# Kernel optimization log

Hardware: AMD Instinct MI355X
Metric: run time of the kernel (lower is better)

Reference implementation:

```python
import jax, jax.numpy as jnp
import numpy as np

EMB = 128     # embedding_size
HEADS = 4     # n_heads
LAYERS = 2    # n_layers
T = 10        # number of graphs / timesteps (== window_size)
N = 20000     # nodes per graph
E = 320000    # edges per graph
B = 4096      # clf_nodes
WIN = 10      # window_size
NEG_SLOPE = 0.2


def setup_inputs() -> dict:
    key = jax.random.key(0)
    ks = jax.random.split(key, 26)
    p = lambda k, shape: 0.05 * jax.random.normal(k, shape, jnp.float32)
    inp = {
        "embeddings": jax.random.normal(ks[0], (T, N, EMB), jnp.float32),
        "edges": jax.random.randint(ks[1], (T, 2, E), 0, N),
        "node_type": jax.random.randint(ks[2], (T, N), 0, 4),
        "edge_type": jax.random.randint(ks[3], (T, E), 0, 4),
        "clf_neighbors": jax.random.randint(ks[4], (B,), 0, N),
        "clf_nodes": jax.random.randint(ks[5], (B,), 0, N),
        # branch 1 GAT stacks: lin weight [L, H*C, D], attention vecs [L, H, C], bias [L, H*C]
        "gat_W1": p(ks[6], (LAYERS, HEADS * EMB, EMB)),
        "gat_as1": p(ks[7], (LAYERS, HEADS, EMB)),
        "gat_ad1": p(ks[8], (LAYERS, HEADS, EMB)),
        "gat_b1": p(ks[9], (LAYERS, HEADS * EMB)),
        "lin_W1": p(ks[10], (LAYERS, EMB, HEADS * EMB)),
        "lin_b1": p(ks[11], (LAYERS, EMB)),
        # branch 2
        "gat_W2": p(ks[12], (LAYERS, HEADS * EMB, EMB)),
        "gat_as2": p(ks[13], (LAYERS, HEADS, EMB)),
        "gat_ad2": p(ks[14], (LAYERS, HEADS, EMB)),
        "gat_b2": p(ks[15], (LAYERS, HEADS * EMB)),
        "lin_W2": p(ks[16], (LAYERS, EMB, HEADS * EMB)),
        "lin_b2": p(ks[17], (LAYERS, EMB)),
        # head MLP (fc1 consumes flattened [window * 2*D])
        "fc1_W": p(ks[18], (EMB, 2 * EMB * WIN)),
        "fc1_b": p(ks[19], (EMB,)),
        "fc2_W": p(ks[20], (2, EMB)),
        "fc2_b": p(ks[21], (2,)),
    }
    return inp


def _gat(x, src, dst, W, a_s, a_d, b):
    """PyG-style GATConv (concat=True, self-loops already in src/dst, eval mode)."""
    n = x.shape[0]
    h = (x @ W.T).reshape(n, HEADS, EMB)                       # [N,H,C]
    logits = jax.nn.leaky_relu((h * a_s).sum(-1)[src] + (h * a_d).sum(-1)[dst], NEG_SLOPE)  # [Etot,H]
    logits = logits - jax.ops.segment_max(logits, dst, num_segments=n)[dst]
    ex = jnp.exp(logits)
    alpha = ex / jax.ops.segment_sum(ex, dst, num_segments=n)[dst]  # segment softmax over targets
    out = jax.ops.segment_sum(alpha[:, :, None] * h[src], dst, num_segments=n)  # [N,H,C]
    return out.reshape(n, HEADS * EMB) + b


def _branch(embeddings, edges, gW, gas, gad, gb, lW, lb):
    loops = jnp.arange(N)

    def step(carry, inputs):
        x, edge = inputs
        src = jnp.concatenate([edge[0], loops])  # add self loops (PyG default)
        dst = jnp.concatenate([edge[1], loops])
        for i in range(LAYERS):
            x = _gat(x, src, dst, gW[i], gas[i], gad[i], gb[i])
            x = jax.nn.relu(x @ lW[i].T + lb[i])
        return carry, x

    _, outs = jax.lax.scan(step, 0, (embeddings, edges))
    return outs  # [T,N,EMB]


def reference(embeddings, edges, node_type, edge_type, clf_neighbors, clf_nodes,
              gat_W1, gat_as1, gat_ad1, gat_b1, lin_W1, lin_b1,
              gat_W2, gat_as2, gat_ad2, gat_b2, lin_W2, lin_b2,
              fc1_W, fc1_b, fc2_W, fc2_b):
    o1 = _branch(embeddings, edges, gat_W1, gat_as1, gat_ad1, gat_b1, lin_W1, lin_b1)
    o2 = _branch(embeddings, edges, gat_W2, gat_as2, gat_ad2, gat_b2, lin_W2, lin_b2)
    # original prepends each graph's output -> reversed timestep order
    e1 = o1[::-1][:, clf_nodes].transpose(1, 0, 2)  # [B,T,EMB]
    e2 = o2[::-1][:, clf_nodes].transpose(1, 0, 2)
    temp = jnp.concatenate([e1, e2], axis=2)        # [B,T,2*EMB]
    # slen == window_size -> skip buffer is fully filled by temp
    flat = temp.reshape(temp.shape[0], WIN * 2 * EMB)
    h = jax.nn.relu(flat @ fc1_W.T + fc1_b)
    return jax.nn.relu(h @ fc2_W.T + fc2_b)        # [B,2]
```

## Files before the change

### kernel.cpp

```cpp
#include <hip/hip_runtime.h>
#include <cstdint>

#define NNODES 20000
#define NEDGES 320000
#define ETOT   340000
#define TSTEPS 10
#define BCLF   4096
#define EMB    128
#define HC     512
#define NEG_SLOPE 0.2f

#define NSB    64
#define SBSPAN 313
#define PCAP   6912
#define ECHUNK 2048
#define NCHUNKS ((NEDGES + ECHUNK - 1) / ECHUNK)
#define NSCHUNK ((NNODES + 255) / 256)
#define STAGECAP 7424

typedef _Float16 half_t;
typedef __attribute__((ext_vector_type(8))) _Float16 half8;
typedef __attribute__((ext_vector_type(4))) float floatx4;

__global__ void cvt_split_kernel(const float* __restrict__ in,
                                 half_t* __restrict__ hi, half_t* __restrict__ lo, long n4) {
    long i = (long)blockIdx.x * 256 + threadIdx.x;
    if (i >= n4) return;
    float4 v = *(const float4*)&in[i * 4];
    half_t h[4], l[4];
    h[0] = (half_t)v.x; l[0] = (half_t)(v.x - (float)h[0]);
    h[1] = (half_t)v.y; l[1] = (half_t)(v.y - (float)h[1]);
    h[2] = (half_t)v.z; l[2] = (half_t)(v.z - (float)h[2]);
    h[3] = (half_t)v.w; l[3] = (half_t)(v.w - (float)h[3]);
    *(unsigned long long*)&hi[i * 4] = *(unsigned long long*)h;
    *(unsigned long long*)&lo[i * 4] = *(unsigned long long*)l;
}

__global__ __launch_bounds__(256) void part64_kernel(const int* __restrict__ edges,
                                                     int* __restrict__ bcnt,
                                                     int* __restrict__ pairs) {
    int g = blockIdx.y;
    int c = blockIdx.x;
    __shared__ int hist[NSB], gbase[NSB], cur[NSB];
    if (threadIdx.x < NSB) hist[threadIdx.x] = 0;
    __syncthreads();
    const int* srcp = edges + (long)g * 2 * NEDGES;
    const int* dstp = srcp + NEDGES;
    int e0 = c * ECHUNK + threadIdx.x;
    int s[8], d[8], sb[8];
#pragma unroll
    for (int i = 0; i < 8; i++) {
        int e = e0 + i * 256;
        if (e < NEDGES) {
            s[i] = srcp[e];
            d[i] = dstp[e];
            sb[i] = (int)((unsigned)d[i] / (unsigned)SBSPAN);
            atomicAdd(&hist[sb[i]], 1);
        } else sb[i] = -1;
    }
    __syncthreads();
    if (threadIdx.x < NSB) {
        int h = hist[threadIdx.x];
        gbase[threadIdx.x] = h ? atomicAdd(&bcnt[g * NSB + threadIdx.x], h) : 0;
        cur[threadIdx.x] = 0;
    }
    __syncthreads();
#pragma unroll
    for (int i = 0; i < 8; i++) {
        if (sb[i] >= 0) {
            int pos = gbase[sb[i]] + atomicAdd(&cur[sb[i]], 1);
            int v = s[i] | ((d[i] - sb[i] * SBSPAN) << 15);
            pairs[((long)(g * NSB + sb[i])) * PCAP + pos] = v;
        }
    }
}

__global__ __launch_bounds__(256) void count_sb_kernel(const int* __restrict__ pairs,
                                                       const int* __restrict__ bcnt,
                                                       int* __restrict__ counts) {
    int g = blockIdx.x >> 6, sb = blockIdx.x & 63;
    __shared__ int hist[SBSPAN];
    for (int i = threadIdx.x; i < SBSPAN; i += 256) hist[i] = 0;
    __syncthreads();
    int n0 = sb * SBSPAN;
    int cnt = bcnt[g * NSB + sb];
    const int* p = pairs + (long)(g * NSB + sb) * PCAP;
    for (int k = threadIdx.x; k < cnt; k += 256)
        atomicAdd(&hist[p[k] >> 15], 1);
    __syncthreads();
    int nn = min(SBSPAN, NNODES - n0);
    for (int i = threadIdx.x; i < nn; i += 256)
        counts[g * NNODES + n0 + i] = hist[i];
}

__global__ void scanA_kernel(const int* __restrict__ counts, int* __restrict__ bsum) {
    int g = blockIdx.x / NSCHUNK, ch = blockIdx.x % NSCHUNK;
    int i = ch * 256 + threadIdx.x;
    int v = (i < NNODES) ? counts[g * NNODES + i] + 1 : 0;
    for (int off = 32; off; off >>= 1) v += __shfl_down(v, off);
    __shared__ int ws[4];
    if ((threadIdx.x & 63) == 0) ws[threadIdx.x >> 6] = v;
    __syncthreads();
    if (threadIdx.x == 0) bsum[blockIdx.x] = ws[0] + ws[1] + ws[2] + ws[3];
}

__global__ void scanB_kernel(const int* __restrict__ bsum, int* __restrict__ boff,
                             int* __restrict__ rowptr) {
    int g = blockIdx.x;
    int tid = threadIdx.x;
    int v = (tid < NSCHUNK) ? bsum[g * NSCHUNK + tid] : 0;
    __shared__ int buf[128];
    buf[tid] = v;
    __syncthreads();
    for (int off = 1; off < 128; off <<= 1) {
        int t = (tid >= off) ? buf[tid - off] : 0;
        __syncthreads();
        buf[tid] += t;
        __syncthreads();
    }
    if (tid < NSCHUNK) boff[g * NSCHUNK + tid] = buf[tid] - v;
    if (tid == 127) rowptr[g * (NNODES + 1) + NNODES] = buf[127];
}

__global__ void scanC_kernel(const int* __restrict__ counts, const int* __restrict__ boff,
                             int* __restrict__ rowptr) {
    int g = blockIdx.x / NSCHUNK, ch = blockIdx.x % NSCHUNK;
    int tid = threadIdx.x;
    int i = ch * 256 + tid;
    int v = (i < NNODES) ? counts[g * NNODES + i] + 1 : 0;
    __shared__ int buf[256];
    buf[tid] = v;
    __syncthreads();
    for (int off = 1; off < 256; off <<= 1) {
        int t = (tid >= off) ? buf[tid - off] : 0;
        __syncthreads();
        buf[tid] += t;
        __syncthreads();
    }
    int excl = boff[blockIdx.x] + buf[tid] - v;
    if (i < NNODES) rowptr[g * (NNODES + 1) + i] = excl;
}

__global__ __launch_bounds__(256) void fill_sb_kernel(const int* __restrict__ pairs,
                                                      const int* __restrict__ bcnt,
                                                      const int* __restrict__ rowptr,
                                                      int* __restrict__ csr_src) {
    int g = blockIdx.x >> 6, sb = blockIdx.x & 63;
    __shared__ int cur[SBSPAN];
    __shared__ int stage[STAGECAP];
    int n0 = sb * SBSPAN;
    int nn = min(SBSPAN, NNODES - n0);
    const int* rp = rowptr + g * (NNODES + 1);
    int base = rp[n0];
    int span = rp[n0 + nn] - base;
    for (int i = threadIdx.x; i < nn; i += 256) {
        int rb = rp[n0 + i] - base;
        stage[rb] = n0 + i;
        cur[i] = rb + 1;
    }
    __syncthreads();
    int cnt = bcnt[g * NSB + sb];
    const int* p = pairs + (long)(g * NSB + sb) * PCAP;
    for (int k = threadIdx.x; k < cnt; k += 256) {
        int v = p[k];
        int pos = atomicAdd(&cur[v >> 15], 1);
        stage[pos] = v & 0x7fff;
    }
    __syncthreads();
    int* dst = csr_src + (long)g * ETOT + base;
    for (int k = threadIdx.x; k < span; k += 256) dst[k] = stage[k];
}

__global__ void prep_was_kernel(const float* __restrict__ W1, const float* __restrict__ W2,
                                const float* __restrict__ as1, const float* __restrict__ as2,
                                const float* __restrict__ ad1, const float* __restrict__ ad2,
                                float* __restrict__ was, float* __restrict__ wad) {
    int b = blockIdx.x;
    int l = b >> 3, z = (b >> 2) & 1, h = b & 3;
    int k = threadIdx.x;
    const float* W  = z ? W2 : W1;
    const float* av = z ? as2 : as1;
    const float* dv = z ? ad2 : ad1;
    float s = 0.f, d = 0.f;
    for (int c = 0; c < 128; c++) {
        float w = W[(long)l * HC * EMB + (h * 128 + c) * 128 + k];
        s = fmaf(w, av[(l * 4 + h) * 128 + c], s);
        d = fmaf(w, dv[(l * 4 + h) * 128 + c], d);
    }
    long idx = ((l * 2 + z) * 4 + h) * 128 + k;
    was[idx] = s;
    wad[idx] = d;
}

__global__ void pack_ws_kernel(const float* __restrict__ wasb, const float* __restrict__ wadb,
                               half_t* __restrict__ WS0h, half_t* __restrict__ WS0l,
                               half_t* __restrict__ WS1h, half_t* __restrict__ WS1l) {
    int b = blockIdx.x;
    int k = threadIdx.x;
    if (b < 16) {
        int z = b >> 3, d = (b >> 2) & 1, h = b & 3;
        const float* src = d ? wadb : wasb;
        float v = src[((long)z * 4 + h) * 128 + k];
        half_t hi = (half_t)v;
        WS0h[b * 128 + k] = hi;
        WS0l[b * 128 + k] = (half_t)(v - (float)hi);
    } else {
        int b2 = b - 16;
        int z = b2 >> 4, r = b2 & 15;
        float v = 0.f;
        if (r < 8) {
            int d = r >> 2, h = r & 3;
            const float* src = d ? wadb : wasb;
            v = src[((long)(2 + z) * 4 + h) * 128 + k];
        }
        half_t hi = (half_t)v;
        WS1h[(z * 16 + r) * 128 + k] = hi;
        WS1l[(z * 16 + r) * 128 + k] = (half_t)(v - (float)hi);
    }
}

__global__ void prep_M_kernel(const float* __restrict__ gW1, const float* __restrict__ gW2,
                              const float* __restrict__ lW1, const float* __restrict__ lW2,
                              half_t* __restrict__ Mh, half_t* __restrict__ Ml) {
    int k = blockIdx.x;
    int inst = blockIdx.y;
    int l = inst >> 1, z = inst & 1;
    int c = threadIdx.x;
    const float* gW = (z ? gW2 : gW1) + (long)l * HC * EMB;
    const float* lW = (z ? lW2 : lW1) + (long)l * EMB * HC;
    float acc[4] = {0.f, 0.f, 0.f, 0.f};
    for (int cp = 0; cp < 128; cp++) {
#pragma unroll
        for (int h = 0; h < 4; h++) {
            float lw = lW[(long)k * 512 + h * 128 + cp];
            float gw = gW[(long)(h * 128 + cp) * 128 + c];
            acc[h] = fmaf(lw, gw, acc[h]);
        }
    }
#pragma unroll
    for (int h = 0; h < 4; h++) {
        long o = ((long)inst * 128 + k) * 512 + h * 128 + c;
        half_t hi = (half_t)acc[h];
        Mh[o] = hi;
        Ml[o] = (half_t)(acc[h] - (float)hi);
    }
}

__global__ void prep_cb_kernel(const float* __restrict__ lW1, const float* __restrict__ lW2,
                               const float* __restrict__ gb1_, const float* __restrict__ gb2_,
                               const float* __restrict__ lb1_, const float* __restrict__ lb2_,
                               float* __restrict__ cb) {
    int inst = blockIdx.x;
    int l = inst >> 1, z = inst & 1;
    int k = threadIdx.x;
    const float* lW = (z ? lW2 : lW1) + (long)l * EMB * HC;
    const float* gb = (z ? gb2_ : gb1_) + l * HC;
    const float* lb = (z ? lb2_ : lb1_) + l * EMB;
    float a = lb[k];
    for (int j = 0; j < 512; j++) a = fmaf(lW[(long)k * 512 + j], gb[j], a);
    cb[inst * 128 + k] = a;
}

__global__ __launch_bounds__(256) void scores_b(
    const half_t* __restrict__ Ahb, const half_t* __restrict__ Alb, long aInst,
    const half_t* __restrict__ WShb, const half_t* __restrict__ WSlb, long wInst, int wMask,
    float* __restrict__ outb, long oInst, int M, int OS, int CMAX) {
    int iy = blockIdx.y;
    const half_t* Ah = Ahb + (long)iy * aInst;
    const half_t* Al = Alb + (long)iy * aInst;
    const half_t* WSh = WShb + (long)(iy & wMask) * wInst;
    const half_t* WSl = WSlb + (long)(iy & wMask) * wInst;
    float* out = outb + (long)iy * oInst;
    __shared__ half_t Bh[16 * 128];
    __shared__ half_t Bl[16 * 128];
    int tid = threadIdx.x;
    *(half8*)&Bh[tid * 8] = *(const half8*)&WSh[tid * 8];
    *(half8*)&Bl[tid * 8] = *(const half8*)&WSl[tid * 8];
    __syncthreads();
    int wave = tid >> 6, lane = tid & 63;
    int l16 = lane & 15, chunk = lane >> 4;
    int r0 = blockIdx.x * 64 + wave * 16;
    int rowc = r0 + l16; if (rowc > M - 1) rowc = M - 1;
    floatx4 acc = (floatx4)0.f;
#pragma unroll
    for (int ko = 0; ko < 128; ko += 32) {
        half8 ah = *(const half8*)&Ah[(long)rowc * 128 + ko + chunk * 8];
        half8 al = *(const half8*)&Al[(long)rowc * 128 + ko + chunk * 8];
        half8 bh = *(const half8*)&Bh[l16 * 128 + ko + chunk * 8];
        half8 bl = *(const half8*)&Bl[l16 * 128 + ko + chunk * 8];
        acc = __builtin_amdgcn_mfma_f32_16x16x32_f16(ah, bh, acc, 0, 0, 0);
        acc = __builtin_amdgcn_mfma_f32_16x16x32_f16(ah, bl, acc, 0, 0, 0);
        acc = __builtin_amdgcn_mfma_f32_16x16x32_f16(al, bh, acc, 0, 0, 0);
    }
#pragma unroll
    for (int reg = 0; reg < 4; reg++) {
        int rr = r0 + chunk * 4 + reg;
        if (rr < M && l16 < CMAX) out[(long)rr * OS + l16] = acc[reg];
    }
}

__global__ __launch_bounds__(256) void agg_x_kernel(
    const half_t* __restrict__ Xb, long xsT, long xsG,
    const float* __restrict__ ssb, int stsh, long ssT, long ssG, int zcol,
    const int* __restrict__ rowptr, const int* __restrict__ csr_src,
    half_t* __restrict__ Yh, half_t* __restrict__ Yl, int t0) {
    int tz = blockIdx.z, t = t0 + tz, z = blockIdx.y;
    int gz = tz * 2 + z;
    int n = blockIdx.x * 4 + (threadIdx.x >> 6);
    int lane = threadIdx.x & 63;
    int h = lane >> 4, cg = lane & 15;
    const int* rp = rowptr + t * (NNODES + 1);
    int beg = rp[n], end = rp[n + 1];
    const int* cs = csr_src + (long)t * ETOT;
    const half_t* Xz = Xb + (long)t * xsT + (long)gz * xsG;
    const float* sz = ssb + (long)t * ssT + (long)gz * ssG + (long)z * zcol;
    float sd = sz[((long)n << stsh) + 4 + h];
    float acc[8];
#pragma unroll
    for (int c = 0; c < 8; c++) acc[c] = 0.f;
    float den = 0.f;

    auto proc4 = [&](int s0, int s1, int s2, int s3) {
        float v0 = sz[((long)s0 << stsh) + h];
        float v1 = sz[((long)s1 << stsh) + h];
        float v2 = sz[((long)s2 << stsh) + h];
        float v3 = sz[((long)s3 << stsh) + h];
        half8 x0 = *(const half8*)&Xz[(long)s0 * 128 + cg * 8];
        half8 x1 = *(const half8*)&Xz[(long)s1 * 128 + cg * 8];
        half8 x2 = *(const half8*)&Xz[(long)s2 * 128 + cg * 8];
        half8 x3 = *(const half8*)&Xz[(long)s3 * 128 + cg * 8];
        float L0 = v0 + sd, L1 = v1 + sd, L2 = v2 + sd, L3 = v3 + sd;
        float w0 = __expf(fmaxf(L0, NEG_SLOPE * L0));
        float w1 = __expf(fmaxf(L1, NEG_SLOPE * L1));
        float w2 = __expf(fmaxf(L2, NEG_SLOPE * L2));
        float w3 = __expf(fmaxf(L3, NEG_SLOPE * L3));
        den += (w0 + w1) + (w2 + w3);
#pragma unroll
        for (int c = 0; c < 8; c++) {
            float a = acc[c];
            a = fmaf(w0, (float)x0[c], a);
            a = fmaf(w1, (float)x1[c], a);
            a = fmaf(w2, (float)x2[c], a);
            a = fmaf(w3, (float)x3[c], a);
            acc[c] = a;
        }
    };

    int j = beg;
    int rem = end - beg;
    if (rem >= 8) {
        int a0 = cs[j], a1 = cs[j + 1], a2 = cs[j + 2], a3 = cs[j + 3];
        while (j + 8 <= end) {
            int b0 = cs[j + 4], b1 = cs[j + 5], b2 = cs[j + 6], b3 = cs[j + 7];
            proc4(a0, a1, a2, a3);
            a0 = b0; a1 = b1; a2 = b2; a3 = b3;
            j += 4;
        }
        proc4(a0, a1, a2, a3);
        j += 4;
    } else if (rem >= 4) {
        proc4(cs[j], cs[j + 1], cs[j + 2], cs[j + 3]);
        j += 4;
    }
    for (; j < end; j++) {
        int src = cs[j];
        float sv = sz[((long)src << stsh) + h];
        half8 x = *(const half8*)&Xz[(long)src * 128 + cg * 8];
        float L = sv + sd;
        float w = __expf(fmaxf(L, NEG_SLOPE * L));
        den += w;
#pragma unroll
        for (int c = 0; c < 8; c++) acc[c] = fmaf(w, (float)x[c], acc[c]);
    }
    float inv = 1.0f / den;
    half8 oh, ol;
#pragma unroll
    for (int c = 0; c < 8; c++) {
        float v = acc[c] * inv;
        half_t hi = (half_t)v;
        oh[c] = hi;
        ol[c] = (half_t)(v - (float)hi);
    }
    long yb = ((long)gz * NNODES + n) * 512 + h * 128 + cg * 8;
    *(half8*)&Yh[yb] = oh;
    *(half8*)&Yl[yb] = ol;
}

__global__ __launch_bounds__(256) void gemm_b(
    const half_t* __restrict__ Ahb, const half_t* __restrict__ Alb, long aInst,
    const half_t* __restrict__ Bhb, const half_t* __restrict__ Blb, long bInst,
    const float* __restrict__ biasb, long biasInst,
    half_t* __restrict__ Ch, half_t* __restrict__ Cl,
    long cInst, int M, int N, int K) {
    const int i = blockIdx.z;
    const half_t* __restrict__ Ah = Ahb + (long)i * aInst;
    const half_t* __restrict__ Al = Alb + (long)i * aInst;
    const half_t* __restrict__ Bh = Bhb + (long)(i & 1) * bInst;
    const half_t* __restrict__ Bl = Blb + (long)(i & 1) * bInst;
    const float* __restrict__ bias = biasb + (long)(i & 1) * biasInst;

    __shared__ half_t Ash[4 * 128 * 8];
    __shared__ half_t Asl[4 * 128 * 8];
    __shared__ half_t Bsh[4 * 128 * 8];
    __shared__ half_t Bsl[4 * 128 * 8];

    const int tid = threadIdx.x;
    const int row0 = blockIdx.x * 128;
    const int col0 = blockIdx.y * 128;
    const int wave = tid >> 6;
    const int lane = tid & 63;
    const int wm = (wave >> 1) * 64;
    const int wn = (wave & 1) * 64;
    const int chunk = lane >> 4;
    const int l16 = lane & 15;

    floatx4 acc[4][4];
#pragma unroll
    for (int ii = 0; ii < 4; ii++)
#pragma unroll
        for (int j = 0; j < 4; j++) acc[ii][j] = (floatx4)0.0f;

    for (int k0 = 0; k0 < K; k0 += 32) {
        __syncthreads();
#pragma unroll
        for (int p = 0; p < 2; p++) {
            int idx = p * 256 + tid;
            int r = idx >> 2, kc = idx & 3;
            int arow = row0 + r;
            half8 vah, val;
            if (arow < M) {
                vah = *(const half8*)&Ah[(long)arow * K + k0 + kc * 8];
                val = *(const half8*)&Al[(long)arow * K + k0 + kc * 8];
            } else {
#pragma unroll
                for (int q = 0; q < 8; q++) { vah[q] = (half_t)0.f; val[q] = (half_t)0.f; }
            }
            *(half8*)&Ash[(kc * 128 + r) * 8] = vah;
            *(half8*)&Asl[(kc * 128 + r) * 8] = val;
            long boff = (long)(col0 + r) * K + k0 + kc * 8;
            *(half8*)&Bsh[(kc * 128 + r) * 8] = *(const half8*)&Bh[boff];
            *(half8*)&Bsl[(kc * 128 + r) * 8] = *(const half8*)&Bl[boff];
        }
        __syncthreads();
        half8 afh[4], afl[4], bfh[4], bfl[4];
#pragma unroll
        for (int mi = 0; mi < 4; mi++) {
            int o = (chunk * 128 + wm + mi * 16 + l16) * 8;
            afh[mi] = *(const half8*)&Ash[o];
            afl[mi] = *(const half8*)&Asl[o];
        }
#pragma unroll
        for (int ni = 0; ni < 4; ni++) {
            int o = (chunk * 128 + wn + ni * 16 + l16) * 8;
            bfh[ni] = *(const half8*)&Bsh[o];
            bfl[ni] = *(const half8*)&Bsl[o];
        }
#pragma unroll
        for (int mi = 0; mi < 4; mi++)
#pragma unroll
            for (int ni = 0; ni < 4; ni++) {
                acc[mi][ni] = __builtin_amdgcn_mfma_f32_16x16x32_f16(
                    afh[mi], bfh[ni], acc[mi][ni], 0, 0, 0);
                acc[mi][ni] = __builtin_amdgcn_mfma_f32_16x16x32_f16(
                    afh[mi], bfl[ni], acc[mi][ni], 0, 0, 0);
                acc[mi][ni] = __builtin_amdgcn_mfma_f32_16x16x32_f16(
                    afl[mi], bfh[ni], acc[mi][ni], 0, 0, 0);
            }
    }

    const int r4 = (lane >> 4) * 4;
#pragma unroll
    for (int mi = 0; mi < 4; mi++) {
#pragma unroll
        for (int reg = 0; reg < 4; reg++) {
            int row = row0 + wm + mi * 16 + r4 + reg;
            if (row >= M) continue;
#pragma unroll
            for (int ni = 0; ni < 4; ni++) {
                int col = col0 + wn + ni * 16 + l16;
                float v = fmaxf(acc[mi][ni][reg] + bias[col], 0.f);
                long o = (long)i * cInst + (long)row * N + col;
                half_t hi = (half_t)v;
                Ch[o] = hi;
                Cl[o] = (half_t)(v - (float)hi);
            }
        }
    }
}

__global__ __launch_bounds__(256) void fc1_part_kernel(
    const half_t* __restrict__ Ah, const half_t* __restrict__ Al,
    const half_t* __restrict__ Bh, const half_t* __restrict__ Bl,
    float* __restrict__ pbuf, int M, int N, int K, int kslice) {
    const int ks = blockIdx.y;
    const int kbeg = ks * kslice;
    const int kend = kbeg + kslice;

    __shared__ half_t Ash[4 * 128 * 8];
    __shared__ half_t Asl[4 * 128 * 8];
    __shared__ half_t Bsh[4 * 128 * 8];
    __shared__ half_t Bsl[4 * 128 * 8];

    const int tid = threadIdx.x;
    const int row0 = blockIdx.x * 128;
    const int wave = tid >> 6;
    const int lane = tid & 63;
    const int wm = (wave >> 1) * 64;
    const int wn = (wave & 1) * 64;
    const int chunk = lane >> 4;
    const int l16 = lane & 15;

    floatx4 acc[4][4];
#pragma unroll
    for (int ii = 0; ii < 4; ii++)
#pragma unroll
        for (int j = 0; j < 4; j++) acc[ii][j] = (floatx4)0.0f;

    for (int k0 = kbeg; k0 < kend; k0 += 32) {
        __syncthreads();
#pragma unroll
        for (int p = 0; p < 2; p++) {
            int idx = p * 256 + tid;
            int r = idx >> 2, kc = idx & 3;
            long aoff = (long)(row0 + r) * K + k0 + kc * 8;
            *(half8*)&Ash[(kc * 128 + r) * 8] = *(const half8*)&Ah[aoff];
            *(half8*)&Asl[(kc * 128 + r) * 8] = *(const half8*)&Al[aoff];
            long boff = (long)r * K + k0 + kc * 8;
            *(half8*)&Bsh[(kc * 128 + r) * 8] = *(const half8*)&Bh[boff];
            *(half8*)&Bsl[(kc * 128 + r) * 8] = *(const half8*)&Bl[boff];
        }
        __syncthreads();
        half8 afh[4], afl[4], bfh[4], bfl[4];
#pragma unroll
        for (int mi = 0; mi < 4; mi++) {
            int o = (chunk * 128 + wm + mi * 16 + l16) * 8;
            afh[mi] = *(const half8*)&Ash[o];
            afl[mi] = *(const half8*)&Asl[o];
        }
#pragma unroll
        for (int ni = 0; ni < 4; ni++) {
            int o = (chunk * 128 + wn + ni * 16 + l16) * 8;
            bfh[ni] = *(const half8*)&Bsh[o];
            bfl[ni] = *(const half8*)&Bsl[o];
        }
#pragma unroll
        for (int mi = 0; mi < 4; mi++)
#pragma unroll
            for (int ni = 0; ni < 4; ni++) {
                acc[mi][ni] = __builtin_amdgcn_mfma_f32_16x16x32_f16(
                    afh[mi], bfh[ni], acc[mi][ni], 0, 0, 0);
                acc[mi][ni] = __builtin_amdgcn_mfma_f32_16x16x32_f16(
                    afh[mi], bfl[ni], acc[mi][ni], 0, 0, 0);
                acc[mi][ni] = __builtin_amdgcn_mfma_f32_16x16x32_f16(
                    afl[mi], bfh[ni], acc[mi][ni], 0, 0, 0);
            }
    }

    const int r4 = (lane >> 4) * 4;
#pragma unroll
    for (int mi = 0; mi < 4; mi++)
#pragma unroll
        for (int reg = 0; reg < 4; reg++) {
            int row = row0 + wm + mi * 16 + r4 + reg;
#pragma unroll
            for (int ni = 0; ni < 4; ni++) {
                int col = wn + ni * 16 + l16;
                pbuf[((long)ks * M + row) * N + col] = acc[mi][ni][reg];
            }
        }
}

__global__ void fc1_reduce_kernel(const float* __restrict__ pbuf, const float* __restrict__ bias,
                                  float* __restrict__ h1, int MN, int KS) {
    int i = blockIdx.x * 256 + threadIdx.x;
    if (i >= MN) return;
    float a = 0.f;
    for (int ks = 0; ks < KS; ks++) a += pbuf[(long)ks * MN + i];
    h1[i] = fmaxf(a + bias[i & (EMB - 1)], 0.f);
}

__global__ void gather_kernel(const half_t* __restrict__ Xh, const half_t* __restrict__ Xl,
                              const int* __restrict__ clf,
                              half_t* __restrict__ flath, half_t* __restrict__ flatl, int t0) {
    int b = blockIdx.x;
    int z = blockIdx.y;
    int tz = blockIdx.z;
    int t = t0 + tz, gz = tz * 2 + z;
    int j = threadIdx.x;
    int node = clf[b];
    long dst = (long)b * (TSTEPS * 2 * EMB) + (TSTEPS - 1 - t) * (2 * EMB) + z * EMB;
    long src = ((long)gz * NNODES + node) * EMB;
    ((unsigned int*)&flath[dst])[j] = ((const unsigned int*)&Xh[src])[j];
    ((unsigned int*)&flatl[dst])[j] = ((const unsigned int*)&Xl[src])[j];
}

__global__ void fc2_kernel(const float* __restrict__ h1, const float* __restrict__ W,
                           const float* __restrict__ bias, float* __restrict__ out) {
    int row = blockIdx.x;
    int lane = threadIdx.x;
    float x0 = h1[(long)row * 128 + lane];
    float x1 = h1[(long)row * 128 + 64 + lane];
    float p0 = x0 * W[lane] + x1 * W[64 + lane];
    float p1 = x0 * W[128 + lane] + x1 * W[192 + lane];
    for (int off = 32; off; off >>= 1) {
        p0 += __shfl_down(p0, off);
        p1 += __shfl_down(p1, off);
    }
    if (lane == 0) {
        out[row * 2 + 0] = fmaxf(p0 + bias[0], 0.f);
        out[row * 2 + 1] = fmaxf(p1 + bias[1], 0.f);
    }
}

extern "C" void kernel_launch(void* const* d_in, const int* in_sizes, int n_in,
                              void* d_out, int out_size, void* d_ws, size_t ws_size,
                              hipStream_t stream) {
    const float* emb     = (const float*)d_in[0];
    const int*   edges   = (const int*)d_in[1];
    const int*   clf     = (const int*)d_in[5];
    const float* gat_W1  = (const float*)d_in[6];
    const float* gat_as1 = (const float*)d_in[7];
    const float* gat_ad1 = (const float*)d_in[8];
    const float* gat_b1  = (const float*)d_in[9];
    const float* lin_W1  = (const float*)d_in[10];
    const float* lin_b1  = (const float*)d_in[11];
    const float* gat_W2  = (const float*)d_in[12];
    const float* gat_as2 = (const float*)d_in[13];
    const float* gat_ad2 = (const float*)d_in[14];
    const float* gat_b2  = (const float*)d_in[15];
    const float* lin_W2  = (const float*)d_in[16];
    const float* lin_b2  = (const float*)d_in[17];
    const float* fc1_W   = (const float*)d_in[18];
    const float* fc1_b   = (const float*)d_in[19];
    const float* fc2_W   = (const float*)d_in[20];
    const float* fc2_b   = (const float*)d_in[21];
    float* out = (float*)d_out;

    char* ws = (char*)d_ws;
    size_t off = 0;
    auto alloc = [&](size_t bytes) -> char* {
        char* p = ws + off;
        off += (bytes + 255) & ~(size_t)255;
        return p;
    };
    int* counts  = (int*)alloc((size_t)TSTEPS * NNODES * 4);
    int* rowptr  = (int*)alloc((size_t)TSTEPS * (NNODES + 1) * 4);
    int* csr_src = (int*)alloc((size_t)TSTEPS * ETOT * 4);
    int* bsum    = (int*)alloc((size_t)TSTEPS * NSCHUNK * 4);
    int* boff    = (int*)alloc((size_t)TSTEPS * NSCHUNK * 4);
    int* bcnt    = (int*)alloc((size_t)TSTEPS * NSB * 4);
    half_t* embh = (half_t*)alloc((size_t)TSTEPS * NNODES * EMB * 2);
    half_t* Mh   = (half_t*)alloc((size_t)4 * EMB * HC * 2);
    half_t* Ml   = (half_t*)alloc((size_t)4 * EMB * HC * 2);
    float*  cb   = (float*)alloc((size_t)4 * EMB * 4);
    half_t* fc1Wh = (half_t*)alloc((size_t)EMB * 2 * EMB * TSTEPS * 2);
    half_t* fc1Wl = (half_t*)alloc((size_t)EMB * 2 * EMB * TSTEPS * 2);
    float* wasb = (float*)alloc((size_t)2 * 2 * 4 * 128 * 4);
    float* wadb = (float*)alloc((size_t)2 * 2 * 4 * 128 * 4);
    half_t* WS0h = (half_t*)alloc((size_t)16 * 128 * 2);
    half_t* WS0l = (half_t*)alloc((size_t)16 * 128 * 2);
    half_t* WS1h = (half_t*)alloc((size_t)2 * 16 * 128 * 2);
    half_t* WS1l = (half_t*)alloc((size_t)2 * 16 * 128 * 2);
    float* s0buf = (float*)alloc((size_t)TSTEPS * NNODES * 16 * 4);
    half_t* flath = (half_t*)alloc((size_t)BCLF * (TSTEPS * 2 * EMB) * 2);
    half_t* flatl = (half_t*)alloc((size_t)BCLF * (TSTEPS * 2 * EMB) * 2);
    float* h1buf = (float*)alloc((size_t)BCLF * EMB * 4);

    size_t region_base = off;
    half_t* embl = (half_t*)alloc((size_t)TSTEPS * NNODES * EMB * 2);
    int* pairs   = (int*)alloc((size_t)TSTEPS * NSB * PCAP * 4);

    const size_t perT = ((size_t)2 * NNODES * HC * 2 * 2) +
                        ((size_t)2 * NNODES * EMB * 2 * 2) +
                        ((size_t)2 * NNODES * 8 * 4) + 2048;
    int TG = 1;
    if (ws_size > region_base + perT) {
        size_t cap = (ws_size - region_base) / perT;
        TG = (cap >= 10) ? 10 : (int)cap;
        if (TG < 1) TG = 1;
    }
    off = region_base;
    half_t* Yh = (half_t*)alloc((size_t)TG * 2 * NNODES * HC * 2);
    half_t* Yl = (half_t*)alloc((size_t)TG * 2 * NNODES * HC * 2);
    half_t* Xh = (half_t*)alloc((size_t)TG * 2 * NNODES * EMB * 2);
    half_t* Xl = (half_t*)alloc((size_t)TG * 2 * NNODES * EMB * 2);
    float* s1buf = (float*)alloc((size_t)TG * 2 * NNODES * 8 * 4);

    {
        long n4 = (long)TSTEPS * NNODES * EMB / 4;
        cvt_split_kernel<<<(int)((n4 + 255) / 256), 256, 0, stream>>>(emb, embh, embl, n4);
        long f4 = (long)EMB * 2 * EMB * TSTEPS / 4;
        cvt_split_kernel<<<(int)((f4 + 255) / 256), 256, 0, stream>>>(fc1_W, fc1Wh, fc1Wl, f4);
    }
    prep_was_kernel<<<16, 128, 0, stream>>>(gat_W1, gat_W2, gat_as1, gat_as2,
                                            gat_ad1, gat_ad2, wasb, wadb);
    pack_ws_kernel<<<48, 128, 0, stream>>>(wasb, wadb, WS0h, WS0l, WS1h, WS1l);
    prep_M_kernel<<<dim3(128, 4), 128, 0, stream>>>(gat_W1, gat_W2, lin_W1, lin_W2, Mh, Ml);
    prep_cb_kernel<<<4, 128, 0, stream>>>(lin_W1, lin_W2, gat_b1, gat_b2, lin_b1, lin_b2, cb);

    scores_b<<<dim3(3125, 1), 256, 0, stream>>>(
        embh, embl, 0, WS0h, WS0l, 0, 0, s0buf, 0, TSTEPS * NNODES, 16, 16);

    hipMemsetAsync(bcnt, 0, (size_t)TSTEPS * NSB * 4, stream);
    part64_kernel<<<dim3(NCHUNKS, TSTEPS), 256, 0, stream>>>(edges, bcnt, pairs);
    count_sb_kernel<<<NSB * TSTEPS, 256, 0, stream>>>(pairs, bcnt, counts);
    scanA_kernel<<<TSTEPS * NSCHUNK, 256, 0, stream>>>(counts, bsum);
    scanB_kernel<<<TSTEPS, 128, 0, stream>>>(bsum, boff, rowptr);
    scanC_kernel<<<TSTEPS * NSCHUNK, 256, 0, stream>>>(counts, boff, rowptr);
    fill_sb_kernel<<<NSB * TSTEPS, 256, 0, stream>>>(pairs, bcnt, rowptr, csr_src);

    for (int t0 = 0; t0 < TSTEPS; t0 += TG) {
        int tg = (TSTEPS - t0 < TG) ? (TSTEPS - t0) : TG;
        agg_x_kernel<<<dim3(5000, 2, tg), 256, 0, stream>>>(
            embh, (long)NNODES * EMB, 0L,
            s0buf, 4, (long)NNODES * 16, 0L, 8,
            rowptr, csr_src, Yh, Yl, t0);
        gemm_b<<<dim3(157, 1, 2 * tg), 256, 0, stream>>>(
            Yh, Yl, (long)NNODES * HC,
            Mh, Ml, (long)EMB * HC, cb, EMB,
            Xh, Xl, (long)NNODES * EMB, NNODES, EMB, HC);
        scores_b<<<dim3(313, 2 * tg), 256, 0, stream>>>(
            Xh, Xl, (long)NNODES * EMB,
            WS1h, WS1l, (long)16 * 128, 1,
            s1buf, (long)NNODES * 8, NNODES, 8, 8);
        agg_x_kernel<<<dim3(5000, 2, tg), 256, 0, stream>>>(
            Xh, 0L, (long)NNODES * EMB,
            s1buf, 3, 0L, (long)NNODES * 8, 0,
            rowptr, csr_src, Yh, Yl, t0);
        gemm_b<<<dim3(157, 1, 2 * tg), 256, 0, stream>>>(
            Yh, Yl, (long)NNODES * HC,
            Mh + (long)2 * EMB * HC, Ml + (long)2 * EMB * HC, (long)EMB * HC,
            cb + 2 * EMB, EMB,
            Xh, Xl, (long)NNODES * EMB, NNODES, EMB, HC);
        gather_kernel<<<dim3(BCLF, 2, tg), 64, 0, stream>>>(Xh, Xl, clf, flath, flatl, t0);
    }
    float* pbuf = (float*)Yh;
    fc1_part_kernel<<<dim3(32, 8), 256, 0, stream>>>(
        flath, flatl, fc1Wh, fc1Wl, pbuf, BCLF, EMB, TSTEPS * 2 * EMB, (TSTEPS * 2 * EMB) / 8);
    fc1_reduce_kernel<<<(BCLF * EMB + 255) / 256, 256, 0, stream>>>(
        pbuf, fc1_b, h1buf, BCLF * EMB, 8);
    fc2_kernel<<<BCLF, 64, 0, stream>>>(h1buf, fc2_W, fc2_b, out);
}
```

Before: 1.770 ms.

## Fuse both branches' GAT aggregation into one kernel sharing CSR traversal

Replaces the per-branch aggregation kernel (grid dimension over two branches) with a templated kernel that processes both branches in one thread, sharing the rowptr/csr_src reads and, for layer one, the shared embedding row loads. The unroll factor drops from 4 to 2 edges per step to keep register pressure manageable with doubled accumulators. This is meant to halve index traffic and, in layer one, halve feature gathers, at the cost of more registers per thread and half as many blocks.

```diff
diff --git a/kernel.cpp b/kernel.cpp
--- a/kernel.cpp
+++ b/kernel.cpp
@@ -299,91 +299,112 @@
     }
 }
 
-__global__ __launch_bounds__(256) void agg_x_kernel(
-    const half_t* __restrict__ Xb, long xsT, long xsG,
-    const float* __restrict__ ssb, int stsh, long ssT, long ssG, int zcol,
+template <bool SX>
+__global__ __launch_bounds__(256) void agg2_kernel(
+    const half_t* __restrict__ X0b, const half_t* __restrict__ X1b, long xsT,
+    const float* __restrict__ sAb, const float* __restrict__ sBb, int stsh, long ssT,
     const int* __restrict__ rowptr, const int* __restrict__ csr_src,
     half_t* __restrict__ Yh, half_t* __restrict__ Yl, int t0) {
-    int tz = blockIdx.z, t = t0 + tz, z = blockIdx.y;
-    int gz = tz * 2 + z;
+    int tz = blockIdx.y, t = t0 + tz;
     int n = blockIdx.x * 4 + (threadIdx.x >> 6);
     int lane = threadIdx.x & 63;
     int h = lane >> 4, cg = lane & 15;
     const int* rp = rowptr + t * (NNODES + 1);
     int beg = rp[n], end = rp[n + 1];
     const int* cs = csr_src + (long)t * ETOT;
-    const half_t* Xz = Xb + (long)t * xsT + (long)gz * xsG;
-    const float* sz = ssb + (long)t * ssT + (long)gz * ssG + (long)z * zcol;
-    float sd = sz[((long)n << stsh) + 4 + h];
-    float acc[8];
-#pragma unroll
-    for (int c = 0; c < 8; c++) acc[c] = 0.f;
-    float den = 0.f;
-
-    auto proc4 = [&](int s0, int s1, int s2, int s3) {
-        float v0 = sz[((long)s0 << stsh) + h];
-        float v1 = sz[((long)s1 << stsh) + h];
-        float v2 = sz[((long)s2 << stsh) + h];
-        float v3 = sz[((long)s3 << stsh) + h];
-        half8 x0 = *(const half8*)&Xz[(long)s0 * 128 + cg * 8];
-        half8 x1 = *(const half8*)&Xz[(long)s1 * 128 + cg * 8];
-        half8 x2 = *(const half8*)&Xz[(long)s2 * 128 + cg * 8];
-        half8 x3 = *(const half8*)&Xz[(long)s3 * 128 + cg * 8];
-        float L0 = v0 + sd, L1 = v1 + sd, L2 = v2 + sd, L3 = v3 + sd;
-        float w0 = __expf(fmaxf(L0, NEG_SLOPE * L0));
-        float w1 = __expf(fmaxf(L1, NEG_SLOPE * L1));
-        float w2 = __expf(fmaxf(L2, NEG_SLOPE * L2));
-        float w3 = __expf(fmaxf(L3, NEG_SLOPE * L3));
-        den += (w0 + w1) + (w2 + w3);
+    const half_t* X0 = X0b + (long)tz * xsT;
+    const half_t* X1 = SX ? X0 : (X1b + (long)tz * xsT);
+    const float* sA = sAb + (long)tz * ssT;
+    const float* sB = sBb + (long)tz * ssT;
+    float sd0 = sA[((long)n << stsh) + 4 + h];
+    float sd1 = sB[((long)n << stsh) + 4 + h];
+    float acc0[8], acc1[8];
+#pragma unroll
+    for (int c = 0; c < 8; c++) { acc0[c] = 0.f; acc1[c] = 0.f; }
+    float den0 = 0.f, den1 = 0.f;
+
+    auto proc2 = [&](int s0, int s1) {
+        float va0 = sA[((long)s0 << stsh) + h];
+        float vb0 = sB[((long)s0 << stsh) + h];
+        float va1 = sA[((long)s1 << stsh) + h];
+        float vb1 = sB[((long)s1 << stsh) + h];
+        half8 xa0 = *(const half8*)&X0[(long)s0 * 128 + cg * 8];
+        half8 xa1 = *(const half8*)&X0[(long)s1 * 128 + cg * 8];
+        half8 xb0, xb1;
+        if (!SX) {
+            xb0 = *(const half8*)&X1[(long)s0 * 128 + cg * 8];
+            xb1 = *(const half8*)&X1[(long)s1 * 128 + cg * 8];
+        }
+        float La0 = va0 + sd0, Lb0 = vb0 + sd1;
+        float La1 = va1 + sd0, Lb1 = vb1 + sd1;
+        float wa0 = __expf(fmaxf(La0, NEG_SLOPE * La0));
+        float wb0 = __expf(fmaxf(Lb0, NEG_SLOPE * Lb0));
+        float wa1 = __expf(fmaxf(La1, NEG_SLOPE * La1));
+        float wb1 = __expf(fmaxf(Lb1, NEG_SLOPE * Lb1));
+        den0 += wa0 + wa1;
+        den1 += wb0 + wb1;
 #pragma unroll
         for (int c = 0; c < 8; c++) {
-            float a = acc[c];
-            a = fmaf(w0, (float)x0[c], a);
-            a = fmaf(w1, (float)x1[c], a);
-            a = fmaf(w2, (float)x2[c], a);
-            a = fmaf(w3, (float)x3[c], a);
-            acc[c] = a;
+            float a = acc0[c];
+            a = fmaf(wa0, (float)xa0[c], a);
+            a = fmaf(wa1, (float)xa1[c], a);
+            acc0[c] = a;
+            float b = acc1[c];
+            b = fmaf(wb0, (float)(SX ? xa0[c] : xb0[c]), b);
+            b = fmaf(wb1, (float)(SX ? xa1[c] : xb1[c]), b);
+            acc1[c] = b;
         }
     };
 
     int j = beg;
-    int rem = end - beg;
-    if (rem >= 8) {
-        int a0 = cs[j], a1 = cs[j + 1], a2 = cs[j + 2], a3 = cs[j + 3];
-        while (j + 8 <= end) {
-            int b0 = cs[j + 4], b1 = cs[j + 5], b2 = cs[j + 6], b3 = cs[j + 7];
-            proc4(a0, a1, a2, a3);
-            a0 = b0; a1 = b1; a2 = b2; a3 = b3;
-            j += 4;
-        }
-        proc4(a0, a1, a2, a3);
-        j += 4;
-    } else if (rem >= 4) {
-        proc4(cs[j], cs[j + 1], cs[j + 2], cs[j + 3]);
-        j += 4;
+    if (end - beg >= 4) {
+        int a0 = cs[j], a1 = cs[j + 1];
+        while (j + 4 <= end) {
+            int b0 = cs[j + 2], b1 = cs[j + 3];
+            proc2(a0, a1);
+            a0 = b0; a1 = b1;
+            j += 2;
+        }
+        proc2(a0, a1);
+        j += 2;
     }
     for (; j < end; j++) {
         int src = cs[j];
-        float sv = sz[((long)src << stsh) + h];
-        half8 x = *(const half8*)&Xz[(long)src * 128 + cg * 8];
-        float L = sv + sd;
-        float w = __expf(fmaxf(L, NEG_SLOPE * L));
-        den += w;
-#pragma unroll
-        for (int c = 0; c < 8; c++) acc[c] = fmaf(w, (float)x[c], acc[c]);
-    }
-    float inv = 1.0f / den;
-    half8 oh, ol;
+        float va = sA[((long)src << stsh) + h];
+        float vb = sB[((long)src << stsh) + h];
+        half8 xa = *(const half8*)&X0[(long)src * 128 + cg * 8];
+        half8 xb;
+        if (!SX) xb = *(const half8*)&X1[(long)src * 128 + cg * 8];
+        float La = va + sd0, Lb = vb + sd1;
+        float wa = __expf(fmaxf(La, NEG_SLOPE * La));
+        float wb = __expf(fmaxf(Lb, NEG_SLOPE * Lb));
+        den0 += wa;
+        den1 += wb;
+#pragma unroll
+        for (int c = 0; c < 8; c++) {
+            acc0[c] = fmaf(wa, (float)xa[c], acc0[c]);
+            acc1[c] = fmaf(wb, (float)(SX ? xa[c] : xb[c]), acc1[c]);
+        }
+    }
+
+    float inv0 = 1.0f / den0;
+    float inv1 = 1.0f / den1;
+    half8 oh0, ol0, oh1, ol1;
 #pragma unroll
     for (int c = 0; c < 8; c++) {
-        float v = acc[c] * inv;
-        half_t hi = (half_t)v;
-        oh[c] = hi;
-        ol[c] = (half_t)(v - (float)hi);
-    }
-    long yb = ((long)gz * NNODES + n) * 512 + h * 128 + cg * 8;
-    *(half8*)&Yh[yb] = oh;
-    *(half8*)&Yl[yb] = ol;
+        float v0 = acc0[c] * inv0;
+        half_t h0 = (half_t)v0;
+        oh0[c] = h0; ol0[c] = (half_t)(v0 - (float)h0);
+        float v1 = acc1[c] * inv1;
+        half_t h1 = (half_t)v1;
+        oh1[c] = h1; ol1[c] = (half_t)(v1 - (float)h1);
+    }
+    long yb0 = ((long)(tz * 2) * NNODES + n) * 512 + h * 128 + cg * 8;
+    long yb1 = yb0 + (long)NNODES * 512;
+    *(half8*)&Yh[yb0] = oh0;
+    *(half8*)&Yl[yb0] = ol0;
+    *(half8*)&Yh[yb1] = oh1;
+    *(half8*)&Yl[yb1] = ol1;
 }
 
 __global__ __launch_bounds__(256) void gemm_b(
@@ -711,9 +732,10 @@
 
     for (int t0 = 0; t0 < TSTEPS; t0 += TG) {
         int tg = (TSTEPS - t0 < TG) ? (TSTEPS - t0) : TG;
-        agg_x_kernel<<<dim3(5000, 2, tg), 256, 0, stream>>>(
-            embh, (long)NNODES * EMB, 0L,
-            s0buf, 4, (long)NNODES * 16, 0L, 8,
+        agg2_kernel<true><<<dim3(5000, tg), 256, 0, stream>>>(
+            embh + (long)t0 * NNODES * EMB, nullptr, (long)NNODES * EMB,
+            s0buf + (long)t0 * NNODES * 16, s0buf + (long)t0 * NNODES * 16 + 8,
+            4, (long)NNODES * 16,
             rowptr, csr_src, Yh, Yl, t0);
         gemm_b<<<dim3(157, 1, 2 * tg), 256, 0, stream>>>(
             Yh, Yl, (long)NNODES * HC,
@@ -723,9 +745,9 @@
             Xh, Xl, (long)NNODES * EMB,
             WS1h, WS1l, (long)16 * 128, 1,
             s1buf, (long)NNODES * 8, NNODES, 8, 8);
-        agg_x_kernel<<<dim3(5000, 2, tg), 256, 0, stream>>>(
-            Xh, 0L, (long)NNODES * EMB,
-            s1buf, 3, 0L, (long)NNODES * 8, 0,
+        agg2_kernel<false><<<dim3(5000, tg), 256, 0, stream>>>(
+            Xh, Xh + (long)NNODES * EMB, (long)2 * NNODES * EMB,
+            s1buf, s1buf + (long)NNODES * 8, 3, (long)2 * NNODES * 8,
             rowptr, csr_src, Yh, Yl, t0);
         gemm_b<<<dim3(157, 1, 2 * tg), 256, 0, stream>>>(
             Yh, Yl, (long)NNODES * HC,
```

Measured after the change: 1.723 ms. 1.03x faster.
